# Kernel tuning notes

Measured on AMD Instinct MI355X. Metric: run time of the kernel, lower is better.

## Reference

```python
import jax, jax.numpy as jnp
import numpy as np

B, P, T = 64, 49, 20      # batch, num_pixels (7x7), caption length
V, E, D, A, ENC = 32000, 512, 512, 512, 2048


def setup_inputs() -> dict:
    key = jax.random.key(0)
    ks = jax.random.split(key, 20)
    s = 0.02
    return {
        "features": jax.random.normal(ks[0], (B, P, ENC), jnp.float32),
        "captions": jax.random.randint(ks[1], (B, T), 0, V, jnp.int64),
        "embed_table": jax.random.normal(ks[2], (V, E), jnp.float32) * s,
        "W_ih": jax.random.normal(ks[3], (4 * D, ENC + E), jnp.float32) * s,
        "b_ih": jnp.zeros((4 * D,), jnp.float32),
        "W_hh": jax.random.normal(ks[4], (4 * D, D), jnp.float32) * s,
        "b_hh": jnp.zeros((4 * D,), jnp.float32),
        "W_init_h": jax.random.normal(ks[5], (ENC, D), jnp.float32) * s,
        "b_init_h": jnp.zeros((D,), jnp.float32),
        "W_init_c": jax.random.normal(ks[6], (ENC, D), jnp.float32) * s,
        "b_init_c": jnp.zeros((D,), jnp.float32),
        "W_enc_att": jax.random.normal(ks[7], (ENC, A), jnp.float32) * s,
        "b_enc_att": jnp.zeros((A,), jnp.float32),
        "W_dec_att": jax.random.normal(ks[8], (D, A), jnp.float32) * s,
        "b_dec_att": jnp.zeros((A,), jnp.float32),
        "w_A": jax.random.normal(ks[9], (A,), jnp.float32) * s,
        "b_A": jnp.zeros((), jnp.float32),
        "W_out": jax.random.normal(ks[10], (D, V), jnp.float32) * s,
        "b_out": jnp.zeros((V,), jnp.float32),
    }


def reference(features, captions, embed_table, W_ih, b_ih, W_hh, b_hh,
              W_init_h, b_init_h, W_init_c, b_init_c,
              W_enc_att, b_enc_att, W_dec_att, b_dec_att, w_A, b_A,
              W_out, b_out):
    # Dropout is treated as identity (eval mode) for a deterministic baseline.
    bsz, seq_len = captions.shape
    emb = embed_table[captions]                              # [B,T,E]
    mean_f = features.mean(axis=1)                           # [B,ENC]
    h0 = mean_f @ W_init_h + b_init_h                        # [B,D]
    c0 = mean_f @ W_init_c + b_init_c                        # [B,D]
    enc_states = features @ W_enc_att + b_enc_att            # [B,P,A] (precomputed, loop-invariant)

    def step(carry, x_t):
        h, c = carry
        dec = h @ W_dec_att + b_dec_att                      # [B,A]
        comb = jnp.tanh(enc_states + dec[:, None, :])        # [B,P,A]
        scores = comb @ w_A + b_A                            # [B,P]
        alpha = jax.nn.softmax(scores, axis=1)
        ctx = jnp.einsum('bpe,bp->be', features, alpha)      # [B,ENC]
        x = jnp.concatenate([ctx, x_t], axis=1)              # [B,ENC+E]
        gates = x @ W_ih.T + b_ih + h @ W_hh.T + b_hh        # [B,4D]
        i, f, g, o = jnp.split(gates, 4, axis=1)
        i, f, o = jax.nn.sigmoid(i), jax.nn.sigmoid(f), jax.nn.sigmoid(o)
        g = jnp.tanh(g)
        c2 = f * c + i * g
        h2 = o * jnp.tanh(c2)
        logits = h2 @ W_out + b_out                          # [B,V]
        return (h2, c2), logits

    xs = jnp.swapaxes(emb[:, :seq_len - 1], 0, 1)            # [T-1,B,E]
    _, preds = jax.lax.scan(step, (h0, c0), xs)              # [T-1,B,V]
    preds = jnp.swapaxes(preds, 0, 1)                        # [B,T-1,V]
    vocab = W_out.shape[1]
    last = jnp.zeros((bsz, 1, vocab), preds.dtype)           # t = T-1 never written
    return jnp.concatenate([preds, last], axis=1)            # [B,T,V]
```

## Files before the change

### kernel.cpp

```cpp
#include <hip/hip_runtime.h>

constexpr int B_   = 64;
constexpr int P_   = 49;
constexpr int T_   = 20;
constexpr int V_   = 32000;
constexpr int E_   = 512;
constexpr int D_   = 512;
constexpr int A_   = 512;
constexpr int ENC_ = 2048;
constexpr int NT_  = T_ - 1;
constexpr int KX_  = ENC_ + E_ + D_;
constexpr int KSPL = 8;
constexpr int GCH  = (KX_ / 64) / KSPL;

#define DI __device__ __forceinline__

using u16 = unsigned short;
typedef short   bf16x8 __attribute__((ext_vector_type(8)));
typedef float   f32x4  __attribute__((ext_vector_type(4)));
typedef u16     u16x4  __attribute__((ext_vector_type(4)));
typedef u16     u16x2  __attribute__((ext_vector_type(2)));

DI float sigm(float x) { return 1.0f / (1.0f + __expf(-x)); }
DI float tanhx(float x) {
  x = fminf(15.0f, fmaxf(-15.0f, x));
  float e = __expf(2.0f * x);
  return (e - 1.0f) / (e + 1.0f);
}
DI u16 f2bf(float x) {
  union { float f; unsigned u; } v{x};
  unsigned r = v.u + 0x7FFF + ((v.u >> 16) & 1);
  return (u16)(r >> 16);
}
DI float bf2f(u16 x) {
  union { unsigned u; float f; } v;
  v.u = ((unsigned)x) << 16;
  return v.f;
}
DI f32x4 mfma16(bf16x8 a, bf16x8 b, f32x4 c) {
  return __builtin_amdgcn_mfma_f32_16x16x32_bf16(a, b, c, 0, 0, 0);
}


__global__ __launch_bounds__(256) void k_mean_bf(const float* __restrict__ feat,
                                                 u16* __restrict__ mfb) {
  int idx = blockIdx.x * 256 + threadIdx.x;
  int b = idx >> 11, e = idx & (ENC_ - 1);
  const float* f = feat + (size_t)b * P_ * ENC_ + e;
  float s = 0.f;
#pragma unroll
  for (int p = 0; p < P_; p++) s += f[(size_t)p * ENC_];
  mfb[idx] = f2bf(s * (1.0f / P_));
}

__global__ __launch_bounds__(256) void k_tr_cvt(const float* __restrict__ in,
    u16* __restrict__ outp, int R, int C) {
  __shared__ float tbuf[32][33];
  int tx = threadIdx.x & 31, ty = threadIdx.x >> 5;
  int c0 = blockIdx.x * 32, r0 = blockIdx.y * 32;
#pragma unroll
  for (int i = 0; i < 4; i++)
    tbuf[ty + 8 * i][tx] = in[(size_t)(r0 + ty + 8 * i) * C + c0 + tx];
  __syncthreads();
#pragma unroll
  for (int i = 0; i < 4; i++)
    outp[(size_t)(c0 + ty + 8 * i) * R + r0 + tx] = f2bf(tbuf[tx][ty + 8 * i]);
}

__global__ __launch_bounds__(256) void k_trW(const float* __restrict__ in,
                                             u16* __restrict__ outp) {
  __shared__ u16 ld[128][264];
  int v0 = blockIdx.x * 128, k0 = blockIdx.y * 256;
  int vf = (threadIdx.x & 31) * 4, kk = threadIdx.x >> 5;
#pragma unroll 4
  for (int p = 0; p < 32; p++) {
    int k = kk + p * 8;
    float4 v = *(const float4*)(in + (size_t)(k0 + k) * V_ + v0 + vf);
    ld[vf + 0][k] = f2bf(v.x);
    ld[vf + 1][k] = f2bf(v.y);
    ld[vf + 2][k] = f2bf(v.z);
    ld[vf + 3][k] = f2bf(v.w);
  }
  __syncthreads();
  int v = threadIdx.x >> 1, h = threadIdx.x & 1;
  u16* op = outp + (size_t)(v0 + v) * D_ + k0 + h * 128;
#pragma unroll
  for (int i = 0; i < 16; i++)
    *(bf16x8*)(op + i * 8) = *(const bf16x8*)(&ld[v][h * 128 + i * 8]);
}

__global__ __launch_bounds__(256) void k_cvt4(const float* __restrict__ in,
                                              u16* __restrict__ o) {
  int i = blockIdx.x * 256 + threadIdx.x;
  float4 v = ((const float4*)in)[i];
  u16x4 r = {f2bf(v.x), f2bf(v.y), f2bf(v.z), f2bf(v.w)};
  ((u16x4*)o)[i] = r;
}

__global__ __launch_bounds__(256) void k_wg4(const float* __restrict__ Wih,
    const float* __restrict__ Whh, u16* __restrict__ Wg) {
  int i = blockIdx.x * 256 + threadIdx.x;
  int j = i / 768, rem = i - j * 768;
  int k = rem * 4;
  const float* src = (k < ENC_ + E_) ? (Wih + (size_t)j * (ENC_ + E_) + k)
                                     : (Whh + (size_t)j * D_ + (k - ENC_ - E_));
  float4 v = *(const float4*)src;
  u16x4 r = {f2bf(v.x), f2bf(v.y), f2bf(v.z), f2bf(v.w)};
  ((u16x4*)Wg)[i] = r;
}

__global__ __launch_bounds__(256) void k_emb_bf(const int* __restrict__ cap,
    const float* __restrict__ tab, u16* __restrict__ embb) {
  int idx = blockIdx.x * 256 + threadIdx.x;
  int e = idx & (E_ - 1);
  int tb = idx >> 9;
  int b = tb & 63, t = tb >> 6;
  embb[idx] = f2bf(tab[(size_t)cap[b * T_ + t] * E_ + e]);
}

__global__ __launch_bounds__(256) void k_zero_last(float* __restrict__ out) {
  int i = blockIdx.x * 256 + threadIdx.x;
  int b = i / 8000, v4 = i - b * 8000;
  float4 z = {0.f, 0.f, 0.f, 0.f};
  *(float4*)(out + ((size_t)b * T_ + (T_ - 1)) * V_ + (size_t)v4 * 4) = z;
}

__global__ __launch_bounds__(256) void k_init_bf(const u16* __restrict__ mfb,
    const u16* __restrict__ WiT, const float* __restrict__ binh,
    const float* __restrict__ binc, u16* __restrict__ hbf, float* __restrict__ c) {
  int wid = threadIdx.x >> 6, lane = threadIdx.x & 63;
  int n0 = blockIdx.x * 64 + wid * 16;
  int l16 = lane & 15, lk = lane >> 4;
  const u16* bp = WiT + (size_t)(n0 + l16) * ENC_ + 8 * lk;
  const u16* ap = mfb + (size_t)l16 * ENC_ + 8 * lk;
  f32x4 acc[4] = {};
#pragma unroll 4
  for (int kc = 0; kc < ENC_; kc += 32) {
    bf16x8 b = *(const bf16x8*)(bp + kc);
#pragma unroll
    for (int mf = 0; mf < 4; mf++) {
      bf16x8 a = *(const bf16x8*)(ap + (size_t)mf * 16 * ENC_ + kc);
      acc[mf] = mfma16(a, b, acc[mf]);
    }
  }
  int n = n0 + l16;
#pragma unroll
  for (int mf = 0; mf < 4; mf++) {
    int m = mf * 16 + 4 * lk;
#pragma unroll
    for (int r = 0; r < 4; r++) {
      float v = acc[mf][r];
      if (n < D_) hbf[(size_t)(m + r) * D_ + n] = f2bf(v + binh[n]);
      else        c[(size_t)(m + r) * D_ + (n - D_)] = v + binc[n - D_];
    }
  }
}


__global__ __launch_bounds__(256) void k_enc_bf(const u16* __restrict__ fb,
    const u16* __restrict__ WeT, const float* __restrict__ benc,
    float* __restrict__ encs) {
  int wid = threadIdx.x >> 6, lane = threadIdx.x & 63;
  int m0 = blockIdx.x * 64, n0 = blockIdx.y * 64 + wid * 16;
  int l16 = lane & 15, lk = lane >> 4;
  const u16* ap = fb + (size_t)(m0 + l16) * ENC_ + 8 * lk;
  const u16* bp = WeT + (size_t)(n0 + l16) * ENC_ + 8 * lk;
  f32x4 acc[4] = {};
#pragma unroll 8
  for (int i = 0; i < ENC_ / 32; i++) {
    int kc = i * 32;
    bf16x8 b = *(const bf16x8*)(bp + kc);
#pragma unroll
    for (int mf = 0; mf < 4; mf++) {
      bf16x8 a = *(const bf16x8*)(ap + (size_t)mf * 16 * ENC_ + kc);
      acc[mf] = mfma16(a, b, acc[mf]);
    }
  }
  float bv = benc[n0 + l16];
#pragma unroll
  for (int mf = 0; mf < 4; mf++) {
    int m = m0 + mf * 16 + 4 * lk;
#pragma unroll
    for (int r = 0; r < 4; r++)
      encs[(size_t)(m + r) * A_ + n0 + l16] = acc[mf][r] + bv;
  }
}

__global__ __launch_bounds__(256) void k_gates_bf(const u16* __restrict__ ctxb,
    const u16* __restrict__ embb, const u16* __restrict__ hbf,
    const u16* __restrict__ Wg, float* __restrict__ gp, int t) {
  int wid = threadIdx.x >> 6, lane = threadIdx.x & 63;
  int j0 = blockIdx.x * 64 + wid * 16;
  int sp = blockIdx.y;
  int l16 = lane & 15, lk = lane >> 4;
  const u16* bp = Wg + (size_t)(j0 + l16) * KX_ + 8 * lk;
  f32x4 acc[4] = {};
#pragma unroll
  for (int i = 0; i < KX_ / KSPL / 32; i++) {
    int kc = sp * (KX_ / KSPL) + i * 32;
    int k = kc + 8 * lk;
    bf16x8 b = *(const bf16x8*)(bp + kc);
#pragma unroll
    for (int mf = 0; mf < 4; mf++) {
      int row = mf * 16 + l16;
      const u16* src;
      if (k < ENC_)            src = ctxb + (size_t)row * ENC_ + k;
      else if (k < ENC_ + E_)  src = embb + ((size_t)t * B_ + row) * E_ + (k - ENC_);
      else                     src = hbf + (size_t)row * D_ + (k - ENC_ - E_);
      bf16x8 a = *(const bf16x8*)src;
      acc[mf] = mfma16(a, b, acc[mf]);
    }
  }
#pragma unroll
  for (int mf = 0; mf < 4; mf++) {
    int m = mf * 16 + 4 * lk;
#pragma unroll
    for (int r = 0; r < 4; r++)
      gp[((size_t)sp * B_ + m + r) * (4 * D_) + j0 + l16] = acc[mf][r];
  }
}

__global__ __launch_bounds__(256) void k_logits_all4(const u16* __restrict__ hall,
    const u16* __restrict__ WoT, const float* __restrict__ bout,
    float* __restrict__ out) {
  __shared__ float tile[64 * 264];
  int L = blockIdx.x;
  int x8 = L & 7, r = L >> 3;
  int g = r / 24, s = r % 24;
  int nt = g * 8 + x8;
  if (nt >= 125 || s >= NT_) return;
  int w = threadIdx.x >> 6, lane = threadIdx.x & 63;
  int l16 = lane & 15, lk = lane >> 4;
  const u16* ap0 = hall + (size_t)s * B_ * D_ + (size_t)l16 * D_ + 8 * lk;
  int ncol0 = nt * 256 + w * 64;
#pragma unroll 1
  for (int ch = 0; ch < 4; ch++) {
    int col = ncol0 + ch * 16 + l16;
    const u16* bp = WoT + (size_t)col * D_ + 8 * lk;
    bf16x8 bfr[16];
#pragma unroll
    for (int kc = 0; kc < 16; kc++) bfr[kc] = *(const bf16x8*)(bp + kc * 32);
    f32x4 acc[4] = {};
#pragma unroll
    for (int kc = 0; kc < 16; kc++) {
#pragma unroll
      for (int mf = 0; mf < 4; mf++) {
        bf16x8 a = *(const bf16x8*)(ap0 + (size_t)mf * 16 * D_ + kc * 32);
        acc[mf] = mfma16(a, bfr[kc], acc[mf]);
      }
    }
    float bv = bout[col];
#pragma unroll
    for (int mf = 0; mf < 4; mf++)
#pragma unroll
      for (int rr = 0; rr < 4; rr++)
        tile[(mf * 16 + 4 * lk + rr) * 264 + w * 64 + ch * 16 + l16] =
            acc[mf][rr] + bv;
  }
  __syncthreads();
  int tr = threadIdx.x >> 2, tc = threadIdx.x & 3;
  float* op = out + ((size_t)tr * T_ + s) * V_ + nt * 256;
  const float* lp = &tile[tr * 264];
#pragma unroll
  for (int j = 0; j < 16; j++) {
    int cc = (tc + j * 4) * 4;
    *(float4*)(op + cc) = *(const float4*)(lp + cc);
  }
}


__global__ __launch_bounds__(512) void k_att3(const u16* __restrict__ featb,
    const float* __restrict__ encs, const u16* __restrict__ WdT,
    const float* __restrict__ bdec, const float* __restrict__ wA,
    const float* __restrict__ bA, const float* __restrict__ gp,
    const float* __restrict__ bih, const float* __restrict__ bhh,
    const float* __restrict__ c_in, float* __restrict__ c_out,
    u16* __restrict__ hbf, u16* __restrict__ hallp, u16* __restrict__ ctxb,
    int do_reduce, int do_att) {
  __shared__ u16 hsb[D_];
  __shared__ float ds[A_];
  __shared__ float sc[P_];
  __shared__ float inv_s;
  int b = blockIdx.x, y = blockIdx.y, tid = threadIdx.x;

  if (do_reduce) {
    int d = tid;
    float g0 = 0, g1 = 0, g2 = 0, g3 = 0;
#pragma unroll
    for (int s = 0; s < KSPL; s++) {
      const float* g = gp + (size_t)(s * B_ + b) * (4 * D_);
      g0 += g[d]; g1 += g[D_ + d]; g2 += g[2 * D_ + d]; g3 += g[3 * D_ + d];
    }
    g0 += bih[d] + bhh[d];
    g1 += bih[D_ + d] + bhh[D_ + d];
    g2 += bih[2 * D_ + d] + bhh[2 * D_ + d];
    g3 += bih[3 * D_ + d] + bhh[3 * D_ + d];
    float iv = sigm(g0), fv = sigm(g1), gv = tanhx(g2), ov = sigm(g3);
    float cv = fmaf(fv, c_in[b * D_ + d], iv * gv);
    float hv = ov * tanhx(cv);
    u16 hb = f2bf(hv);
    hsb[d] = hb;
    if (y == 0) {
      c_out[b * D_ + d] = cv;
      hbf[b * D_ + d] = hb;
      hallp[b * D_ + d] = hb;
    }
  } else {
    hsb[tid] = hbf[b * D_ + tid];
  }
  __syncthreads();
  if (!do_att) return;

  {
    int w = tid >> 6, lane = tid & 63, l16 = lane & 15, lk = lane >> 4;
#pragma unroll
    for (int f = 0; f < 4; f++) {
      int n = w * 64 + f * 16 + l16;
      const u16* bp = WdT + (size_t)n * D_ + 8 * lk;
      f32x4 acc = {};
#pragma unroll
      for (int kc = 0; kc < D_; kc += 32) {
        bf16x8 av = *(const bf16x8*)(hsb + kc + 8 * lk);
        bf16x8 bv = *(const bf16x8*)(bp + kc);
        acc = mfma16(av, bv, acc);
      }
      if (lk == 0) ds[n] = acc[0] + bdec[n];
    }
  }
  __syncthreads();

  int wv_ = tid >> 6, ln = tid & 63;
  float bA0 = bA[0];
  for (int p = wv_; p < P_; p += 8) {
    const float* ep = encs + (size_t)(b * P_ + p) * A_;
    float s = 0.f;
#pragma unroll
    for (int a = ln; a < A_; a += 64) s += tanhx(ep[a] + ds[a]) * wA[a];
#pragma unroll
    for (int off = 32; off; off >>= 1) s += __shfl_down(s, off);
    if (ln == 0) sc[p] = s + bA0;
  }
  __syncthreads();

  if (tid == 0) {
    float mx = -1e30f;
    for (int p = 0; p < P_; p++) mx = fmaxf(mx, sc[p]);
    float sum = 0.f;
    for (int p = 0; p < P_; p++) { float ex = __expf(sc[p] - mx); sc[p] = ex; sum += ex; }
    inv_s = 1.0f / sum;
  }
  __syncthreads();

  {
    float inv = inv_s;
    int e = y * 1024 + tid * 2;
    const u16* fp = featb + (size_t)b * P_ * ENC_ + e;
    float s0 = 0.f, s1 = 0.f;
#pragma unroll
    for (int p = 0; p < P_; p++) {
      u16x2 w = *(const u16x2*)(fp + (size_t)p * ENC_);
      s0 = fmaf(bf2f(w.x), sc[p], s0);
      s1 = fmaf(bf2f(w.y), sc[p], s1);
    }
    u16x2 o = {f2bf(s0 * inv), f2bf(s1 * inv)};
    *(u16x2*)(ctxb + b * ENC_ + e) = o;
  }
}


DI int swz(int row, int slot) { return row * 64 + ((slot ^ (row >> 2)) << 2); }

__global__ __launch_bounds__(256) void k_mean(const float* __restrict__ feat,
                                              float* __restrict__ mf) {
  int idx = blockIdx.x * 256 + threadIdx.x;
  int b = idx >> 11, e = idx & (ENC_ - 1);
  const float* f = feat + (size_t)b * P_ * ENC_ + e;
  float s = 0.f;
#pragma unroll
  for (int p = 0; p < P_; p++) s += f[(size_t)p * ENC_];
  mf[idx] = s * (1.0f / P_);
}

__global__ __launch_bounds__(256) void k_emb(const int* __restrict__ cap,
                                             const float* __restrict__ tab,
                                             float* __restrict__ emb) {
  int idx = blockIdx.x * 256 + threadIdx.x;
  int e  = idx & (E_ - 1);
  int bt = idx >> 9;
  int b = bt / NT_, t = bt - b * NT_;
  int tok = cap[b * T_ + t];
  emb[idx] = tab[(size_t)tok * E_ + e];
}

__global__ __launch_bounds__(256) void k_init(const float* __restrict__ mf,
    const float* __restrict__ Wh, const float* __restrict__ bh,
    const float* __restrict__ Wc, const float* __restrict__ bc,
    float* __restrict__ h, float* __restrict__ c) {
  __shared__ float ms[ENC_];
  int b = blockIdx.y;
  for (int i = threadIdx.x; i < ENC_; i += 256) ms[i] = mf[b * ENC_ + i];
  __syncthreads();
  int d = blockIdx.x * 256 + threadIdx.x;
  const float* W = blockIdx.z ? Wc : Wh;
  float s = (blockIdx.z ? bc : bh)[d];
#pragma unroll 8
  for (int e = 0; e < ENC_; e++) s = fmaf(ms[e], W[(size_t)e * D_ + d], s);
  (blockIdx.z ? c : h)[b * D_ + d] = s;
}

__global__ __launch_bounds__(256) void k_enc(const float* __restrict__ Ag,
    const float* __restrict__ Wg, const float* __restrict__ bias,
    float* __restrict__ Cg) {
  __shared__ float As[64 * 64], Ws[64 * 64];
  int m0 = blockIdx.x * 64, n0 = blockIdx.y * 64;
  int tid = threadIdx.x, tn = tid & 15, tm = tid >> 4;
  float acc[4][4] = {};
#pragma unroll 1
  for (int ch = 0; ch < ENC_ / 64; ch++) {
    int k0 = ch * 64;
    __syncthreads();
#pragma unroll
    for (int q = 0; q < 4; q++) {
      int idx = tid + q * 256;
      int row = idx >> 4, slot = idx & 15;
      *(float4*)&As[swz(row, slot)] =
          *(const float4*)(Ag + (size_t)(m0 + row) * ENC_ + k0 + slot * 4);
      *(float4*)&Ws[swz(row, slot)] =
          *(const float4*)(Wg + (size_t)(k0 + row) * A_ + n0 + slot * 4);
    }
    __syncthreads();
#pragma unroll
    for (int kk = 0; kk < 16; kk++) {
      float4 av[4], wv[4];
#pragma unroll
      for (int i = 0; i < 4; i++) av[i] = *(float4*)&As[swz(4 * tm + i, kk)];
#pragma unroll
      for (int u = 0; u < 4; u++) wv[u] = *(float4*)&Ws[swz(4 * kk + u, tn)];
      const float* wq = (const float*)wv;
#pragma unroll
      for (int i = 0; i < 4; i++) {
        const float* aq = (const float*)&av[i];
#pragma unroll
        for (int j = 0; j < 4; j++) {
          float s = acc[i][j];
#pragma unroll
          for (int u = 0; u < 4; u++) s = fmaf(aq[u], wq[u * 4 + j], s);
          acc[i][j] = s;
        }
      }
    }
  }
#pragma unroll
  for (int i = 0; i < 4; i++) {
    int m = m0 + 4 * tm + i, n = n0 + 4 * tn;
    float4 bv = *(const float4*)(bias + n);
    float4 o = {acc[i][0] + bv.x, acc[i][1] + bv.y, acc[i][2] + bv.z, acc[i][3] + bv.w};
    *(float4*)(Cg + (size_t)m * A_ + n) = o;
  }
}

__global__ __launch_bounds__(256) void k_logits(const float* __restrict__ h,
    const float* __restrict__ Wout, const float* __restrict__ bout,
    float* __restrict__ out, int t) {
  __shared__ float As[64 * 64], Ws[64 * 64];
  int n0 = blockIdx.x * 64;
  int tid = threadIdx.x, tn = tid & 15, tm = tid >> 4;
  float acc[4][4] = {};
#pragma unroll 1
  for (int ch = 0; ch < D_ / 64; ch++) {
    int k0 = ch * 64;
    __syncthreads();
#pragma unroll
    for (int q = 0; q < 4; q++) {
      int idx = tid + q * 256;
      int row = idx >> 4, slot = idx & 15;
      *(float4*)&As[swz(row, slot)] =
          *(const float4*)(h + (size_t)row * D_ + k0 + slot * 4);
      *(float4*)&Ws[swz(row, slot)] =
          *(const float4*)(Wout + (size_t)(k0 + row) * V_ + n0 + slot * 4);
    }
    __syncthreads();
#pragma unroll
    for (int kk = 0; kk < 16; kk++) {
      float4 av[4], wv[4];
#pragma unroll
      for (int i = 0; i < 4; i++) av[i] = *(float4*)&As[swz(4 * tm + i, kk)];
#pragma unroll
      for (int u = 0; u < 4; u++) wv[u] = *(float4*)&Ws[swz(4 * kk + u, tn)];
      const float* wq = (const float*)wv;
#pragma unroll
      for (int i = 0; i < 4; i++) {
        const float* aq = (const float*)&av[i];
#pragma unroll
        for (int j = 0; j < 4; j++) {
          float s = acc[i][j];
#pragma unroll
          for (int u = 0; u < 4; u++) s = fmaf(aq[u], wq[u * 4 + j], s);
          acc[i][j] = s;
        }
      }
    }
  }
#pragma unroll
  for (int i = 0; i < 4; i++) {
    int m = 4 * tm + i, n = n0 + 4 * tn;
    float4 bv = *(const float4*)(bout + n);
    float4 o = {acc[i][0] + bv.x, acc[i][1] + bv.y, acc[i][2] + bv.z, acc[i][3] + bv.w};
    *(float4*)(out + ((size_t)m * T_ + t) * V_ + n) = o;
  }
}

__global__ __launch_bounds__(256) void k_gates(const float* __restrict__ ctx,
    const float* __restrict__ emb, const float* __restrict__ h,
    const float* __restrict__ Wih, const float* __restrict__ Whh,
    float* __restrict__ gp, int t) {
  __shared__ float As[64 * 64], Ws[64 * 64];
  int n0 = blockIdx.x * 64;
  int sp = blockIdx.y;
  int tid = threadIdx.x, tn = tid & 15, tm = tid >> 4;
  float acc[4][4] = {};
#pragma unroll 1
  for (int ch = 0; ch < GCH; ch++) {
    int k0 = sp * (GCH * 64) + ch * 64;
    __syncthreads();
#pragma unroll
    for (int q = 0; q < 4; q++) {
      int idx = tid + q * 256;
      int row = idx >> 4, slot = idx & 15;
      int k = k0 + slot * 4;
      float4 xv;
      if (k < ENC_)            xv = *(const float4*)(ctx + (size_t)row * ENC_ + k);
      else if (k < ENC_ + E_)  xv = *(const float4*)(emb + ((size_t)row * NT_ + t) * E_ + (k - ENC_));
      else                     xv = *(const float4*)(h + (size_t)row * D_ + (k - ENC_ - E_));
      *(float4*)&As[swz(row, slot)] = xv;
      int j = n0 + row;
      float4 wv2;
      if (k < ENC_ + E_) wv2 = *(const float4*)(Wih + (size_t)j * (ENC_ + E_) + k);
      else               wv2 = *(const float4*)(Whh + (size_t)j * D_ + (k - ENC_ - E_));
      *(float4*)&Ws[swz(row, slot)] = wv2;
    }
    __syncthreads();
#pragma unroll
    for (int kk = 0; kk < 16; kk++) {
      float4 av[4], wv[4];
#pragma unroll
      for (int i = 0; i < 4; i++) av[i] = *(float4*)&As[swz(4 * tm + i, kk)];
#pragma unroll
      for (int j = 0; j < 4; j++) wv[j] = *(float4*)&Ws[swz(4 * tn + j, kk)];
#pragma unroll
      for (int i = 0; i < 4; i++) {
        const float* aq = (const float*)&av[i];
#pragma unroll
        for (int j = 0; j < 4; j++) {
          const float* wqj = (const float*)&wv[j];
          float s = acc[i][j];
#pragma unroll
          for (int u = 0; u < 4; u++) s = fmaf(aq[u], wqj[u], s);
          acc[i][j] = s;
        }
      }
    }
  }
#pragma unroll
  for (int i = 0; i < 4; i++) {
    int b = 4 * tm + i, j = n0 + 4 * tn;
    float4 o = {acc[i][0], acc[i][1], acc[i][2], acc[i][3]};
    *(float4*)(gp + ((size_t)(sp * B_ + b)) * (4 * D_) + j) = o;
  }
}

__global__ __launch_bounds__(512) void k_att(const float* __restrict__ feat,
    const float* __restrict__ encs, const float* __restrict__ Wdec,
    const float* __restrict__ bdec, const float* __restrict__ wA,
    const float* __restrict__ bA, const float* __restrict__ gp,
    const float* __restrict__ bih, const float* __restrict__ bhh,
    float* __restrict__ h, float* __restrict__ c, float* __restrict__ ctx,
    int do_reduce, int do_att) {
  __shared__ float hs[D_];
  __shared__ float ds[A_];
  __shared__ float sc[P_];
  __shared__ float inv_s;
  int b = blockIdx.x, tid = threadIdx.x;

  if (do_reduce) {
    int d = tid;
    float g0 = 0, g1 = 0, g2 = 0, g3 = 0;
#pragma unroll
    for (int s = 0; s < KSPL; s++) {
      const float* g = gp + (size_t)(s * B_ + b) * (4 * D_);
      g0 += g[d]; g1 += g[D_ + d]; g2 += g[2 * D_ + d]; g3 += g[3 * D_ + d];
    }
    g0 += bih[d] + bhh[d];
    g1 += bih[D_ + d] + bhh[D_ + d];
    g2 += bih[2 * D_ + d] + bhh[2 * D_ + d];
    g3 += bih[3 * D_ + d] + bhh[3 * D_ + d];
    float iv = sigm(g0), fv = sigm(g1), gv = tanhx(g2), ov = sigm(g3);
    float cv = fmaf(fv, c[b * D_ + d], iv * gv);
    float hv = ov * tanhx(cv);
    c[b * D_ + d] = cv;
    h[b * D_ + d] = hv;
    hs[d] = hv;
  } else {
    hs[tid] = h[b * D_ + tid];
  }
  __syncthreads();
  if (!do_att) return;

  {
    int a = tid;
    float s = bdec[a];
#pragma unroll 8
    for (int d = 0; d < D_; d++) s = fmaf(hs[d], Wdec[(size_t)d * A_ + a], s);
    ds[a] = s;
  }
  __syncthreads();

  int wv_ = tid >> 6, ln = tid & 63;
  float bA0 = bA[0];
  for (int p = wv_; p < P_; p += 8) {
    const float* ep = encs + (size_t)(b * P_ + p) * A_;
    float s = 0.f;
#pragma unroll
    for (int a = ln; a < A_; a += 64) s += tanhx(ep[a] + ds[a]) * wA[a];
#pragma unroll
    for (int off = 32; off; off >>= 1) s += __shfl_down(s, off);
    if (ln == 0) sc[p] = s + bA0;
  }
  __syncthreads();

  if (tid == 0) {
    float mx = -1e30f;
    for (int p = 0; p < P_; p++) mx = fmaxf(mx, sc[p]);
    float sum = 0.f;
    for (int p = 0; p < P_; p++) { float ex = __expf(sc[p] - mx); sc[p] = ex; sum += ex; }
    inv_s = 1.0f / sum;
  }
  __syncthreads();

  float inv = inv_s;
  for (int e = tid; e < ENC_; e += 512) {
    const float* fp = feat + (size_t)b * P_ * ENC_ + e;
    float s = 0.f;
#pragma unroll
    for (int p = 0; p < P_; p++) s = fmaf(fp[(size_t)p * ENC_], sc[p], s);
    ctx[b * ENC_ + e] = s * inv;
  }
}


extern "C" void kernel_launch(void* const* d_in, const int* in_sizes, int n_in,
                              void* d_out, int out_size, void* d_ws, size_t ws_size,
                              hipStream_t stream) {
  const float* features = (const float*)d_in[0];
  const int*   captions = (const int*)d_in[1];
  const float* table    = (const float*)d_in[2];
  const float* Wih  = (const float*)d_in[3];
  const float* bih  = (const float*)d_in[4];
  const float* Whh  = (const float*)d_in[5];
  const float* bhh  = (const float*)d_in[6];
  const float* Winh = (const float*)d_in[7];
  const float* binh = (const float*)d_in[8];
  const float* Winc = (const float*)d_in[9];
  const float* binc = (const float*)d_in[10];
  const float* Wenc = (const float*)d_in[11];
  const float* benc = (const float*)d_in[12];
  const float* Wdec = (const float*)d_in[13];
  const float* bdec = (const float*)d_in[14];
  const float* wA   = (const float*)d_in[15];
  const float* bA   = (const float*)d_in[16];
  const float* Wout = (const float*)d_in[17];
  const float* bout = (const float*)d_in[18];
  float* out = (float*)d_out;

  constexpr size_t F_ENC = (size_t)B_ * P_ * A_;
  constexpr size_t F_C   = (size_t)B_ * D_;
  constexpr size_t F_GP  = (size_t)KSPL * B_ * 4 * D_;
  constexpr size_t U_WOT = (size_t)V_ * D_;
  constexpr size_t U_WG  = (size_t)(4 * D_) * KX_;
  constexpr size_t U_HBF = (size_t)B_ * D_;
  constexpr size_t U_CTX = (size_t)B_ * ENC_;
  constexpr size_t U_FEAT = (size_t)B_ * P_ * ENC_;
  constexpr size_t U_WET = (size_t)A_ * ENC_;
  constexpr size_t U_EMB = (size_t)NT_ * B_ * E_;
  constexpr size_t U_WDT = (size_t)A_ * D_;
  constexpr size_t U_HALL = (size_t)NT_ * B_ * D_;
  static_assert(U_EMB + U_WDT <= U_WET, "embb+WdT overlay WeT region");
  constexpr size_t NEED_BYTES =
      (F_ENC + 2 * F_C + F_GP) * 4 +
      (U_WOT + U_WG + U_HBF + U_CTX + U_FEAT + U_WET + U_HALL) * 2;

  if (ws_size >= NEED_BYTES) {
    float* ws = (float*)d_ws;
    float* enc_states = ws;
    float* cbuf0  = enc_states + F_ENC;
    float* cbuf1  = cbuf0 + F_C;
    float* gparts = cbuf1 + F_C;
    u16* WoT   = (u16*)(gparts + F_GP);
    u16* Wg    = WoT + U_WOT;
    u16* hbf   = Wg + U_WG;
    u16* ctxb  = hbf + U_HBF;
    u16* featb = ctxb + U_CTX;
    u16* wetr  = featb + U_FEAT;
    u16* WeT   = wetr;
    u16* embb  = wetr;
    u16* WdT   = wetr + U_EMB;
    u16* hall  = wetr + U_WET;
    u16* WiT   = (u16*)gparts;
    u16* mfb   = ctxb;
    float* cb[2] = {cbuf0, cbuf1};

    k_mean_bf<<<512, 256, 0, stream>>>(features, mfb);
    k_tr_cvt<<<dim3(D_ / 32, ENC_ / 32), 256, 0, stream>>>(Winh, WiT, ENC_, D_);
    k_tr_cvt<<<dim3(D_ / 32, ENC_ / 32), 256, 0, stream>>>(Winc, WiT + (size_t)D_ * ENC_, ENC_, D_);
    k_init_bf<<<16, 256, 0, stream>>>(mfb, WiT, binh, binc, hbf, cbuf0);
    k_cvt4<<<(int)(U_FEAT / 4 / 256), 256, 0, stream>>>(features, featb);
    k_tr_cvt<<<dim3(A_ / 32, ENC_ / 32), 256, 0, stream>>>(Wenc, WeT, ENC_, A_);
    k_enc_bf<<<dim3(49, 8), 256, 0, stream>>>(featb, WeT, benc, enc_states);
    k_emb_bf<<<2432, 256, 0, stream>>>(captions, table, embb);
    k_tr_cvt<<<dim3(A_ / 32, D_ / 32), 256, 0, stream>>>(Wdec, WdT, D_, A_);
    k_trW<<<dim3(V_ / 128, D_ / 256), 256, 0, stream>>>(Wout, WoT);
    k_wg4<<<(int)(U_WG / 4 / 256), 256, 0, stream>>>(Wih, Whh, Wg);
    k_zero_last<<<2000, 256, 0, stream>>>(out);

    for (int t = 0; t < NT_; t++) {
      u16* hallp = (t > 0) ? (hall + (size_t)(t - 1) * B_ * D_) : hall;
      const float* cin = cb[(t > 0 ? (t - 1) : 0) & 1];
      float* cout = cb[t & 1];
      k_att3<<<dim3(64, 2), 512, 0, stream>>>(featb, enc_states, WdT, bdec, wA,
                                              bA, gparts, bih, bhh, cin, cout,
                                              hbf, hallp, ctxb, t > 0 ? 1 : 0, 1);
      k_gates_bf<<<dim3(32, KSPL), 256, 0, stream>>>(ctxb, embb, hbf, Wg, gparts, t);
    }
    k_att3<<<dim3(64, 1), 512, 0, stream>>>(featb, enc_states, WdT, bdec, wA,
                                            bA, gparts, bih, bhh,
                                            cb[(NT_ - 1) & 1], cb[NT_ & 1], hbf,
                                            hall + (size_t)(NT_ - 1) * B_ * D_,
                                            ctxb, 1, 0);
    k_logits_all4<<<3072, 256, 0, stream>>>(hall, WoT, bout, out);
  } else {
    float* ws = (float*)d_ws;
    float* enc_states = ws;
    float* mean_f = enc_states + (size_t)B_ * P_ * A_;
    float* emb    = mean_f + (size_t)B_ * ENC_;
    float* h      = emb + (size_t)B_ * NT_ * E_;
    float* c      = h + (size_t)B_ * D_;
    float* ctx    = c + (size_t)B_ * D_;
    float* gparts = ctx + (size_t)B_ * ENC_;

    k_mean<<<512, 256, 0, stream>>>(features, mean_f);
    k_emb<<<2432, 256, 0, stream>>>(captions, table, emb);
    k_init<<<dim3(2, 64, 2), 256, 0, stream>>>(mean_f, Winh, binh, Winc, binc, h, c);
    k_enc<<<dim3(49, 8), 256, 0, stream>>>(features, Wenc, benc, enc_states);
    k_zero_last<<<2000, 256, 0, stream>>>(out);

    for (int t = 0; t < NT_; t++) {
      k_att<<<64, 512, 0, stream>>>(features, enc_states, Wdec, bdec, wA, bA,
                                    gparts, bih, bhh, h, c, ctx, t > 0 ? 1 : 0, 1);
      if (t > 0)
        k_logits<<<500, 256, 0, stream>>>(h, Wout, bout, out, t - 1);
      k_gates<<<dim3(32, KSPL), 256, 0, stream>>>(ctx, emb, h, Wih, Whh, gparts, t);
    }
    k_att<<<64, 512, 0, stream>>>(features, enc_states, Wdec, bdec, wA, bA,
                                  gparts, bih, bhh, h, c, ctx, 1, 0);
    k_logits<<<500, 256, 0, stream>>>(h, Wout, bout, out, NT_ - 1);
  }
}
```

Baseline: 1.208 ms.

## Fuse recurrent loop into persistent cooperative kernel overlapping logits with recurrence

```diff
diff --git a/kernel.cpp b/kernel.cpp
--- a/kernel.cpp
+++ b/kernel.cpp
@@ -1,4 +1,7 @@
 #include <hip/hip_runtime.h>
+#include <hip/hip_cooperative_groups.h>
+
+namespace cg = cooperative_groups;
 
 constexpr int B_   = 64;
 constexpr int P_   = 49;
@@ -156,7 +159,6 @@
   }
 }
 
-
 __global__ __launch_bounds__(256) void k_enc_bf(const u16* __restrict__ fb,
     const u16* __restrict__ WeT, const float* __restrict__ benc,
     float* __restrict__ encs) {
@@ -185,6 +187,217 @@
       encs[(size_t)(m + r) * A_ + n0 + l16] = acc[mf][r] + bv;
   }
 }
+
+
+DI void logits_tile_512(int nt, int s, const u16* __restrict__ hall,
+                        const u16* __restrict__ WoT,
+                        const float* __restrict__ bout,
+                        float* __restrict__ out, float* __restrict__ tile) {
+  int tid = threadIdx.x;
+  int w = tid >> 6, lane = tid & 63, l16 = lane & 15, lk = lane >> 4;
+  const u16* ap0 = hall + (size_t)s * B_ * D_ + (size_t)l16 * D_ + 8 * lk;
+#pragma unroll
+  for (int ch = 0; ch < 2; ch++) {
+    int col = nt * 256 + w * 32 + ch * 16 + l16;
+    const u16* bp = WoT + (size_t)col * D_ + 8 * lk;
+    f32x4 acc[4] = {};
+#pragma unroll
+    for (int kc = 0; kc < 16; kc++) {
+      bf16x8 b = *(const bf16x8*)(bp + kc * 32);
+#pragma unroll
+      for (int mf = 0; mf < 4; mf++) {
+        bf16x8 a = *(const bf16x8*)(ap0 + (size_t)mf * 16 * D_ + kc * 32);
+        acc[mf] = mfma16(a, b, acc[mf]);
+      }
+    }
+    float bv = bout[col];
+#pragma unroll
+    for (int mf = 0; mf < 4; mf++)
+#pragma unroll
+      for (int rr = 0; rr < 4; rr++)
+        tile[(mf * 16 + 4 * lk + rr) * 264 + w * 32 + ch * 16 + l16] =
+            acc[mf][rr] + bv;
+  }
+  __syncthreads();
+  int tr = tid >> 3, tc = tid & 7;
+  float* op = out + ((size_t)tr * T_ + s) * V_ + nt * 256;
+  const float* lp = tile + tr * 264;
+#pragma unroll
+  for (int j = 0; j < 8; j++) {
+    int cc = (tc + j * 8) * 4;
+    *(float4*)(op + cc) = *(const float4*)(lp + cc);
+  }
+}
+
+__global__ __launch_bounds__(512) void k_loop(
+    const u16* __restrict__ featb, const float* __restrict__ encs,
+    const u16* __restrict__ WdT, const float* __restrict__ bdec,
+    const float* __restrict__ wA, const float* __restrict__ bA,
+    float* __restrict__ gparts, const float* __restrict__ bih,
+    const float* __restrict__ bhh, float* __restrict__ cbuf,
+    u16* __restrict__ hbf, u16* __restrict__ hall, u16* __restrict__ ctxb,
+    const u16* __restrict__ embb, const u16* __restrict__ Wg,
+    const u16* __restrict__ WoT, const float* __restrict__ bout,
+    float* __restrict__ out) {
+  cg::grid_group grid = cg::this_grid();
+  __shared__ float tile[64 * 264];
+  __shared__ u16 hsb[D_];
+  __shared__ float ds[A_];
+  __shared__ float sc[P_];
+  __shared__ float inv_s;
+  int bid = blockIdx.x, tid = threadIdx.x;
+
+  for (int t = 0; t < NT_; t++) {
+    if (bid < 64) {
+      int b = bid;
+      if (t > 0) {
+        int d = tid;
+        float g0 = 0, g1 = 0, g2 = 0, g3 = 0;
+#pragma unroll
+        for (int s = 0; s < KSPL; s++) {
+          const float* g = gparts + (size_t)(s * B_ + b) * (4 * D_);
+          g0 += g[d]; g1 += g[D_ + d]; g2 += g[2 * D_ + d]; g3 += g[3 * D_ + d];
+        }
+        g0 += bih[d] + bhh[d];
+        g1 += bih[D_ + d] + bhh[D_ + d];
+        g2 += bih[2 * D_ + d] + bhh[2 * D_ + d];
+        g3 += bih[3 * D_ + d] + bhh[3 * D_ + d];
+        float iv = sigm(g0), fv = sigm(g1), gv = tanhx(g2), ov = sigm(g3);
+        float cv = fmaf(fv, cbuf[b * D_ + d], iv * gv);
+        float hv = ov * tanhx(cv);
+        cbuf[b * D_ + d] = cv;
+        u16 hb = f2bf(hv);
+        hsb[d] = hb;
+        hbf[b * D_ + d] = hb;
+        hall[(size_t)(t - 1) * B_ * D_ + b * D_ + d] = hb;
+      } else {
+        hsb[tid] = hbf[b * D_ + tid];
+      }
+      __syncthreads();
+
+      {
+        int w = tid >> 6, lane = tid & 63, l16 = lane & 15, lk = lane >> 4;
+#pragma unroll
+        for (int f = 0; f < 4; f++) {
+          int n = w * 64 + f * 16 + l16;
+          const u16* bp = WdT + (size_t)n * D_ + 8 * lk;
+          f32x4 acc = {};
+#pragma unroll
+          for (int kc = 0; kc < D_; kc += 32) {
+            bf16x8 av = *(const bf16x8*)(hsb + kc + 8 * lk);
+            bf16x8 bv = *(const bf16x8*)(bp + kc);
+            acc = mfma16(av, bv, acc);
+          }
+          if (lk == 0) ds[n] = acc[0] + bdec[n];
+        }
+      }
+      __syncthreads();
+
+      {
+        int wv_ = tid >> 6, ln = tid & 63;
+        float bA0 = bA[0];
+        for (int p = wv_; p < P_; p += 8) {
+          const float* ep = encs + (size_t)(b * P_ + p) * A_;
+          float s = 0.f;
+#pragma unroll
+          for (int a = ln; a < A_; a += 64) s += tanhx(ep[a] + ds[a]) * wA[a];
+#pragma unroll
+          for (int off = 32; off; off >>= 1) s += __shfl_down(s, off);
+          if (ln == 0) sc[p] = s + bA0;
+        }
+      }
+      __syncthreads();
+      if (tid == 0) {
+        float mx = -1e30f;
+        for (int p = 0; p < P_; p++) mx = fmaxf(mx, sc[p]);
+        float sum = 0.f;
+        for (int p = 0; p < P_; p++) { float ex = __expf(sc[p] - mx); sc[p] = ex; sum += ex; }
+        inv_s = 1.0f / sum;
+      }
+      __syncthreads();
+
+      {
+        float inv = inv_s;
+        int e = tid * 4;
+        const u16* fp = featb + (size_t)b * P_ * ENC_ + e;
+        float s0 = 0.f, s1 = 0.f, s2 = 0.f, s3 = 0.f;
+#pragma unroll
+        for (int p = 0; p < P_; p++) {
+          u16x4 w = *(const u16x4*)(fp + (size_t)p * ENC_);
+          float scp = sc[p];
+          s0 = fmaf(bf2f(w.x), scp, s0);
+          s1 = fmaf(bf2f(w.y), scp, s1);
+          s2 = fmaf(bf2f(w.z), scp, s2);
+          s3 = fmaf(bf2f(w.w), scp, s3);
+        }
+        u16x4 o = {f2bf(s0 * inv), f2bf(s1 * inv), f2bf(s2 * inv), f2bf(s3 * inv)};
+        *(u16x4*)(ctxb + b * ENC_ + e) = o;
+      }
+    } else if (t >= 2 && bid - 64 < 125) {
+      logits_tile_512(bid - 64, t - 2, hall, WoT, bout, out, tile);
+    }
+    grid.sync();
+
+    if (bid < 128) {
+      int wid8 = tid >> 6;
+      int ob = bid * 2 + (wid8 >> 2);
+      int wid = wid8 & 3;
+      int lane = tid & 63;
+      int j0 = (ob & 31) * 64 + wid * 16;
+      int sp = ob >> 5;
+      int l16 = lane & 15, lk = lane >> 4;
+      const u16* bp = Wg + (size_t)(j0 + l16) * KX_ + 8 * lk;
+      f32x4 acc[4] = {};
+#pragma unroll
+      for (int i = 0; i < KX_ / KSPL / 32; i++) {
+        int kc = sp * (KX_ / KSPL) + i * 32;
+        int k = kc + 8 * lk;
+        bf16x8 b = *(const bf16x8*)(bp + kc);
+#pragma unroll
+        for (int mf = 0; mf < 4; mf++) {
+          int row = mf * 16 + l16;
+          const u16* src;
+          if (k < ENC_)            src = ctxb + (size_t)row * ENC_ + k;
+          else if (k < ENC_ + E_)  src = embb + ((size_t)t * B_ + row) * E_ + (k - ENC_);
+          else                     src = hbf + (size_t)row * D_ + (k - ENC_ - E_);
+          bf16x8 a = *(const bf16x8*)src;
+          acc[mf] = mfma16(a, b, acc[mf]);
+        }
+      }
+#pragma unroll
+      for (int mf = 0; mf < 4; mf++) {
+        int m = mf * 16 + 4 * lk;
+#pragma unroll
+        for (int r = 0; r < 4; r++)
+          gparts[((size_t)sp * B_ + m + r) * (4 * D_) + j0 + l16] = acc[mf][r];
+      }
+    }
+    grid.sync();
+  }
+
+  if (bid < 64) {
+    int b = bid, d = tid;
+    float g0 = 0, g1 = 0, g2 = 0, g3 = 0;
+#pragma unroll
+    for (int s = 0; s < KSPL; s++) {
+      const float* g = gparts + (size_t)(s * B_ + b) * (4 * D_);
+      g0 += g[d]; g1 += g[D_ + d]; g2 += g[2 * D_ + d]; g3 += g[3 * D_ + d];
+    }
+    g0 += bih[d] + bhh[d];
+    g1 += bih[D_ + d] + bhh[D_ + d];
+    g2 += bih[2 * D_ + d] + bhh[2 * D_ + d];
+    g3 += bih[3 * D_ + d] + bhh[3 * D_ + d];
+    float iv = sigm(g0), fv = sigm(g1), gv = tanhx(g2), ov = sigm(g3);
+    float cv = fmaf(fv, cbuf[b * D_ + d], iv * gv);
+    float hv = ov * tanhx(cv);
+    hall[(size_t)(NT_ - 1) * B_ * D_ + b * D_ + d] = f2bf(hv);
+  } else if (bid - 64 < 125) {
+    logits_tile_512(bid - 64, NT_ - 2, hall, WoT, bout, out, tile);
+  }
+  grid.sync();
+  if (bid < 125) logits_tile_512(bid, NT_ - 1, hall, WoT, bout, out, tile);
+}
+
 
 __global__ __launch_bounds__(256) void k_gates_bf(const u16* __restrict__ ctxb,
     const u16* __restrict__ embb, const u16* __restrict__ hbf,
@@ -237,16 +450,14 @@
   for (int ch = 0; ch < 4; ch++) {
     int col = ncol0 + ch * 16 + l16;
     const u16* bp = WoT + (size_t)col * D_ + 8 * lk;
-    bf16x8 bfr[16];
-#pragma unroll
-    for (int kc = 0; kc < 16; kc++) bfr[kc] = *(const bf16x8*)(bp + kc * 32);
     f32x4 acc[4] = {};
 #pragma unroll
     for (int kc = 0; kc < 16; kc++) {
+      bf16x8 b = *(const bf16x8*)(bp + kc * 32);
 #pragma unroll
       for (int mf = 0; mf < 4; mf++) {
         bf16x8 a = *(const bf16x8*)(ap0 + (size_t)mf * 16 * D_ + kc * 32);
-        acc[mf] = mfma16(a, bfr[kc], acc[mf]);
+        acc[mf] = mfma16(a, b, acc[mf]);
       }
     }
     float bv = bout[col];
@@ -267,7 +478,6 @@
     *(float4*)(op + cc) = *(const float4*)(lp + cc);
   }
 }
-
 
 __global__ __launch_bounds__(512) void k_att3(const u16* __restrict__ featb,
     const float* __restrict__ encs, const u16* __restrict__ WdT,
@@ -707,7 +917,6 @@
     u16* hall  = wetr + U_WET;
     u16* WiT   = (u16*)gparts;
     u16* mfb   = ctxb;
-    float* cb[2] = {cbuf0, cbuf1};
 
     k_mean_bf<<<512, 256, 0, stream>>>(features, mfb);
     k_tr_cvt<<<dim3(D_ / 32, ENC_ / 32), 256, 0, stream>>>(Winh, WiT, ENC_, D_);
@@ -722,21 +931,34 @@
     k_wg4<<<(int)(U_WG / 4 / 256), 256, 0, stream>>>(Wih, Whh, Wg);
     k_zero_last<<<2000, 256, 0, stream>>>(out);
 
-    for (int t = 0; t < NT_; t++) {
-      u16* hallp = (t > 0) ? (hall + (size_t)(t - 1) * B_ * D_) : hall;
-      const float* cin = cb[(t > 0 ? (t - 1) : 0) & 1];
-      float* cout = cb[t & 1];
-      k_att3<<<dim3(64, 2), 512, 0, stream>>>(featb, enc_states, WdT, bdec, wA,
-                                              bA, gparts, bih, bhh, cin, cout,
-                                              hbf, hallp, ctxb, t > 0 ? 1 : 0, 1);
-      k_gates_bf<<<dim3(32, KSPL), 256, 0, stream>>>(ctxb, embb, hbf, Wg, gparts, t);
-    }
-    k_att3<<<dim3(64, 1), 512, 0, stream>>>(featb, enc_states, WdT, bdec, wA,
-                                            bA, gparts, bih, bhh,
-                                            cb[(NT_ - 1) & 1], cb[NT_ & 1], hbf,
-                                            hall + (size_t)(NT_ - 1) * B_ * D_,
-                                            ctxb, 1, 0);
-    k_logits_all4<<<3072, 256, 0, stream>>>(hall, WoT, bout, out);
+    void* kargs[] = {
+        (void*)&featb, (void*)&enc_states, (void*)&WdT, (void*)&bdec,
+        (void*)&wA, (void*)&bA, (void*)&gparts, (void*)&bih, (void*)&bhh,
+        (void*)&cbuf0, (void*)&hbf, (void*)&hall, (void*)&ctxb, (void*)&embb,
+        (void*)&Wg, (void*)&WoT, (void*)&bout, (void*)&out};
+    hipError_t ce = hipLaunchCooperativeKernel((void*)k_loop, dim3(256),
+                                               dim3(512), kargs, 0, stream);
+    if (ce != hipSuccess) {
+      float* cb[2] = {cbuf0, cbuf1};
+      for (int t = 0; t < NT_; t++) {
+        u16* hallp = (t > 0) ? (hall + (size_t)(t - 1) * B_ * D_) : hall;
+        const float* cin = cb[(t > 0 ? (t - 1) : 0) & 1];
+        float* cout = cb[t & 1];
+        k_att3<<<dim3(64, 2), 512, 0, stream>>>(featb, enc_states, WdT, bdec,
+                                                wA, bA, gparts, bih, bhh, cin,
+                                                cout, hbf, hallp, ctxb,
+                                                t > 0 ? 1 : 0, 1);
+        k_gates_bf<<<dim3(32, KSPL), 256, 0, stream>>>(ctxb, embb, hbf, Wg,
+                                                       gparts, t);
+      }
+      k_att3<<<dim3(64, 1), 512, 0, stream>>>(featb, enc_states, WdT, bdec, wA,
+                                              bA, gparts, bih, bhh,
+                                              cb[(NT_ - 1) & 1], cb[NT_ & 1],
+                                              hbf,
+                                              hall + (size_t)(NT_ - 1) * B_ * D_,
+                                              ctxb, 1, 0);
+      k_logits_all4<<<3072, 256, 0, stream>>>(hall, WoT, bout, out);
+    }
   } else {
     float* ws = (float*)d_ws;
     float* enc_states = ws;
```

Measured after the change: 3.476 ms. 2.88x slower.

## Split fused attention step into reduce, decoder-proj and attention kernels; halve gate K-split

Applied to the files above, without the earlier changes.

```diff
diff --git a/kernel.cpp b/kernel.cpp
--- a/kernel.cpp
+++ b/kernel.cpp
@@ -12,6 +12,7 @@
 constexpr int KX_  = ENC_ + E_ + D_;
 constexpr int KSPL = 8;
 constexpr int GCH  = (KX_ / 64) / KSPL;
+constexpr int KS4  = 4;
 
 #define DI __device__ __forceinline__
 
@@ -19,7 +20,6 @@
 typedef short   bf16x8 __attribute__((ext_vector_type(8)));
 typedef float   f32x4  __attribute__((ext_vector_type(4)));
 typedef u16     u16x4  __attribute__((ext_vector_type(4)));
-typedef u16     u16x2  __attribute__((ext_vector_type(2)));
 
 DI float sigm(float x) { return 1.0f / (1.0f + __expf(-x)); }
 DI float tanhx(float x) {
@@ -156,7 +156,6 @@
   }
 }
 
-
 __global__ __launch_bounds__(256) void k_enc_bf(const u16* __restrict__ fb,
     const u16* __restrict__ WeT, const float* __restrict__ benc,
     float* __restrict__ encs) {
@@ -186,7 +185,107 @@
   }
 }
 
-__global__ __launch_bounds__(256) void k_gates_bf(const u16* __restrict__ ctxb,
+
+__global__ __launch_bounds__(512) void k_red(const float* __restrict__ gp,
+    const float* __restrict__ bih, const float* __restrict__ bhh,
+    float* __restrict__ c, u16* __restrict__ hbf, u16* __restrict__ hallp) {
+  int b = blockIdx.x, d = threadIdx.x;
+  float g0 = 0, g1 = 0, g2 = 0, g3 = 0;
+#pragma unroll
+  for (int s = 0; s < KS4; s++) {
+    const float* g = gp + (size_t)(s * B_ + b) * (4 * D_);
+    g0 += g[d]; g1 += g[D_ + d]; g2 += g[2 * D_ + d]; g3 += g[3 * D_ + d];
+  }
+  g0 += bih[d] + bhh[d];
+  g1 += bih[D_ + d] + bhh[D_ + d];
+  g2 += bih[2 * D_ + d] + bhh[2 * D_ + d];
+  g3 += bih[3 * D_ + d] + bhh[3 * D_ + d];
+  float iv = sigm(g0), fv = sigm(g1), gv = tanhx(g2), ov = sigm(g3);
+  float cv = fmaf(fv, c[b * D_ + d], iv * gv);
+  float hv = ov * tanhx(cv);
+  c[b * D_ + d] = cv;
+  u16 hb = f2bf(hv);
+  hbf[b * D_ + d] = hb;
+  hallp[b * D_ + d] = hb;
+}
+
+__global__ __launch_bounds__(256) void k_dec(const u16* __restrict__ hbf,
+    const u16* __restrict__ WdT, const float* __restrict__ bdec,
+    float* __restrict__ dsg) {
+  int wid = threadIdx.x >> 6, lane = threadIdx.x & 63;
+  int n0 = blockIdx.x * 64 + wid * 16;
+  int l16 = lane & 15, lk = lane >> 4;
+  const u16* bp = WdT + (size_t)(n0 + l16) * D_ + 8 * lk;
+  const u16* ap = hbf + (size_t)l16 * D_ + 8 * lk;
+  f32x4 acc[4] = {};
+#pragma unroll
+  for (int kc = 0; kc < D_; kc += 32) {
+    bf16x8 b = *(const bf16x8*)(bp + kc);
+#pragma unroll
+    for (int mf = 0; mf < 4; mf++) {
+      bf16x8 a = *(const bf16x8*)(ap + (size_t)mf * 16 * D_ + kc);
+      acc[mf] = mfma16(a, b, acc[mf]);
+    }
+  }
+  int n = n0 + l16;
+  float bv = bdec[n];
+#pragma unroll
+  for (int mf = 0; mf < 4; mf++) {
+    int m = mf * 16 + 4 * lk;
+#pragma unroll
+    for (int r = 0; r < 4; r++)
+      dsg[(size_t)(m + r) * A_ + n] = acc[mf][r] + bv;
+  }
+}
+
+__global__ __launch_bounds__(512) void k_att4(const float* __restrict__ encs,
+    const float* __restrict__ dsg, const float* __restrict__ wA,
+    const float* __restrict__ bA, const u16* __restrict__ featb,
+    u16* __restrict__ ctxb) {
+  __shared__ float sc[P_];
+  __shared__ float inv_s;
+  int b = blockIdx.x, tid = threadIdx.x;
+  int wv_ = tid >> 6, ln = tid & 63;
+  float bA0 = bA[0];
+  const float* dsb = dsg + (size_t)b * A_;
+  for (int p = wv_; p < P_; p += 8) {
+    const float* ep = encs + (size_t)(b * P_ + p) * A_;
+    float s = 0.f;
+#pragma unroll
+    for (int a = ln; a < A_; a += 64) s += tanhx(ep[a] + dsb[a]) * wA[a];
+#pragma unroll
+    for (int off = 32; off; off >>= 1) s += __shfl_down(s, off);
+    if (ln == 0) sc[p] = s + bA0;
+  }
+  __syncthreads();
+  if (tid == 0) {
+    float mx = -1e30f;
+    for (int p = 0; p < P_; p++) mx = fmaxf(mx, sc[p]);
+    float sum = 0.f;
+    for (int p = 0; p < P_; p++) { float ex = __expf(sc[p] - mx); sc[p] = ex; sum += ex; }
+    inv_s = 1.0f / sum;
+  }
+  __syncthreads();
+  {
+    float inv = inv_s;
+    int e = tid * 4;
+    const u16* fp = featb + (size_t)b * P_ * ENC_ + e;
+    float s0 = 0.f, s1 = 0.f, s2 = 0.f, s3 = 0.f;
+#pragma unroll
+    for (int p = 0; p < P_; p++) {
+      u16x4 w = *(const u16x4*)(fp + (size_t)p * ENC_);
+      float scp = sc[p];
+      s0 = fmaf(bf2f(w.x), scp, s0);
+      s1 = fmaf(bf2f(w.y), scp, s1);
+      s2 = fmaf(bf2f(w.z), scp, s2);
+      s3 = fmaf(bf2f(w.w), scp, s3);
+    }
+    u16x4 o = {f2bf(s0 * inv), f2bf(s1 * inv), f2bf(s2 * inv), f2bf(s3 * inv)};
+    *(u16x4*)(ctxb + b * ENC_ + e) = o;
+  }
+}
+
+__global__ __launch_bounds__(256) void k_gates4(const u16* __restrict__ ctxb,
     const u16* __restrict__ embb, const u16* __restrict__ hbf,
     const u16* __restrict__ Wg, float* __restrict__ gp, int t) {
   int wid = threadIdx.x >> 6, lane = threadIdx.x & 63;
@@ -196,8 +295,8 @@
   const u16* bp = Wg + (size_t)(j0 + l16) * KX_ + 8 * lk;
   f32x4 acc[4] = {};
 #pragma unroll
-  for (int i = 0; i < KX_ / KSPL / 32; i++) {
-    int kc = sp * (KX_ / KSPL) + i * 32;
+  for (int i = 0; i < KX_ / KS4 / 32; i++) {
+    int kc = sp * (KX_ / KS4) + i * 32;
     int k = kc + 8 * lk;
     bf16x8 b = *(const bf16x8*)(bp + kc);
 #pragma unroll
@@ -219,6 +318,7 @@
       gp[((size_t)sp * B_ + m + r) * (4 * D_) + j0 + l16] = acc[mf][r];
   }
 }
+
 
 __global__ __launch_bounds__(256) void k_logits_all4(const u16* __restrict__ hall,
     const u16* __restrict__ WoT, const float* __restrict__ bout,
@@ -237,16 +337,14 @@
   for (int ch = 0; ch < 4; ch++) {
     int col = ncol0 + ch * 16 + l16;
     const u16* bp = WoT + (size_t)col * D_ + 8 * lk;
-    bf16x8 bfr[16];
-#pragma unroll
-    for (int kc = 0; kc < 16; kc++) bfr[kc] = *(const bf16x8*)(bp + kc * 32);
     f32x4 acc[4] = {};
 #pragma unroll
     for (int kc = 0; kc < 16; kc++) {
+      bf16x8 b = *(const bf16x8*)(bp + kc * 32);
 #pragma unroll
       for (int mf = 0; mf < 4; mf++) {
         bf16x8 a = *(const bf16x8*)(ap0 + (size_t)mf * 16 * D_ + kc * 32);
-        acc[mf] = mfma16(a, bfr[kc], acc[mf]);
+        acc[mf] = mfma16(a, b, acc[mf]);
       }
     }
     float bv = bout[col];
@@ -265,105 +363,6 @@
   for (int j = 0; j < 16; j++) {
     int cc = (tc + j * 4) * 4;
     *(float4*)(op + cc) = *(const float4*)(lp + cc);
-  }
-}
-
-
-__global__ __launch_bounds__(512) void k_att3(const u16* __restrict__ featb,
-    const float* __restrict__ encs, const u16* __restrict__ WdT,
-    const float* __restrict__ bdec, const float* __restrict__ wA,
-    const float* __restrict__ bA, const float* __restrict__ gp,
-    const float* __restrict__ bih, const float* __restrict__ bhh,
-    const float* __restrict__ c_in, float* __restrict__ c_out,
-    u16* __restrict__ hbf, u16* __restrict__ hallp, u16* __restrict__ ctxb,
-    int do_reduce, int do_att) {
-  __shared__ u16 hsb[D_];
-  __shared__ float ds[A_];
-  __shared__ float sc[P_];
-  __shared__ float inv_s;
-  int b = blockIdx.x, y = blockIdx.y, tid = threadIdx.x;
-
-  if (do_reduce) {
-    int d = tid;
-    float g0 = 0, g1 = 0, g2 = 0, g3 = 0;
-#pragma unroll
-    for (int s = 0; s < KSPL; s++) {
-      const float* g = gp + (size_t)(s * B_ + b) * (4 * D_);
-      g0 += g[d]; g1 += g[D_ + d]; g2 += g[2 * D_ + d]; g3 += g[3 * D_ + d];
-    }
-    g0 += bih[d] + bhh[d];
-    g1 += bih[D_ + d] + bhh[D_ + d];
-    g2 += bih[2 * D_ + d] + bhh[2 * D_ + d];
-    g3 += bih[3 * D_ + d] + bhh[3 * D_ + d];
-    float iv = sigm(g0), fv = sigm(g1), gv = tanhx(g2), ov = sigm(g3);
-    float cv = fmaf(fv, c_in[b * D_ + d], iv * gv);
-    float hv = ov * tanhx(cv);
-    u16 hb = f2bf(hv);
-    hsb[d] = hb;
-    if (y == 0) {
-      c_out[b * D_ + d] = cv;
-      hbf[b * D_ + d] = hb;
-      hallp[b * D_ + d] = hb;
-    }
-  } else {
-    hsb[tid] = hbf[b * D_ + tid];
-  }
-  __syncthreads();
-  if (!do_att) return;
-
-  {
-    int w = tid >> 6, lane = tid & 63, l16 = lane & 15, lk = lane >> 4;
-#pragma unroll
-    for (int f = 0; f < 4; f++) {
-      int n = w * 64 + f * 16 + l16;
-      const u16* bp = WdT + (size_t)n * D_ + 8 * lk;
-      f32x4 acc = {};
-#pragma unroll
-      for (int kc = 0; kc < D_; kc += 32) {
-        bf16x8 av = *(const bf16x8*)(hsb + kc + 8 * lk);
-        bf16x8 bv = *(const bf16x8*)(bp + kc);
-        acc = mfma16(av, bv, acc);
-      }
-      if (lk == 0) ds[n] = acc[0] + bdec[n];
-    }
-  }
-  __syncthreads();
-
-  int wv_ = tid >> 6, ln = tid & 63;
-  float bA0 = bA[0];
-  for (int p = wv_; p < P_; p += 8) {
-    const float* ep = encs + (size_t)(b * P_ + p) * A_;
-    float s = 0.f;
-#pragma unroll
-    for (int a = ln; a < A_; a += 64) s += tanhx(ep[a] + ds[a]) * wA[a];
-#pragma unroll
-    for (int off = 32; off; off >>= 1) s += __shfl_down(s, off);
-    if (ln == 0) sc[p] = s + bA0;
-  }
-  __syncthreads();
-
-  if (tid == 0) {
-    float mx = -1e30f;
-    for (int p = 0; p < P_; p++) mx = fmaxf(mx, sc[p]);
-    float sum = 0.f;
-    for (int p = 0; p < P_; p++) { float ex = __expf(sc[p] - mx); sc[p] = ex; sum += ex; }
-    inv_s = 1.0f / sum;
-  }
-  __syncthreads();
-
-  {
-    float inv = inv_s;
-    int e = y * 1024 + tid * 2;
-    const u16* fp = featb + (size_t)b * P_ * ENC_ + e;
-    float s0 = 0.f, s1 = 0.f;
-#pragma unroll
-    for (int p = 0; p < P_; p++) {
-      u16x2 w = *(const u16x2*)(fp + (size_t)p * ENC_);
-      s0 = fmaf(bf2f(w.x), sc[p], s0);
-      s1 = fmaf(bf2f(w.y), sc[p], s1);
-    }
-    u16x2 o = {f2bf(s0 * inv), f2bf(s1 * inv)};
-    *(u16x2*)(ctxb + b * ENC_ + e) = o;
   }
 }
 
@@ -685,6 +684,8 @@
   constexpr size_t U_WDT = (size_t)A_ * D_;
   constexpr size_t U_HALL = (size_t)NT_ * B_ * D_;
   static_assert(U_EMB + U_WDT <= U_WET, "embb+WdT overlay WeT region");
+  static_assert((size_t)KS4 * B_ * 4 * D_ + (size_t)B_ * A_ <= F_GP,
+                "gp(KS4)+dsg fit in gparts region");
   constexpr size_t NEED_BYTES =
       (F_ENC + 2 * F_C + F_GP) * 4 +
       (U_WOT + U_WG + U_HBF + U_CTX + U_FEAT + U_WET + U_HALL) * 2;
@@ -695,6 +696,7 @@
     float* cbuf0  = enc_states + F_ENC;
     float* cbuf1  = cbuf0 + F_C;
     float* gparts = cbuf1 + F_C;
+    float* dsg    = gparts + (size_t)KS4 * B_ * 4 * D_;
     u16* WoT   = (u16*)(gparts + F_GP);
     u16* Wg    = WoT + U_WOT;
     u16* hbf   = Wg + U_WG;
@@ -707,7 +709,6 @@
     u16* hall  = wetr + U_WET;
     u16* WiT   = (u16*)gparts;
     u16* mfb   = ctxb;
-    float* cb[2] = {cbuf0, cbuf1};
 
     k_mean_bf<<<512, 256, 0, stream>>>(features, mfb);
     k_tr_cvt<<<dim3(D_ / 32, ENC_ / 32), 256, 0, stream>>>(Winh, WiT, ENC_, D_);
@@ -723,19 +724,15 @@
     k_zero_last<<<2000, 256, 0, stream>>>(out);
 
     for (int t = 0; t < NT_; t++) {
-      u16* hallp = (t > 0) ? (hall + (size_t)(t - 1) * B_ * D_) : hall;
-      const float* cin = cb[(t > 0 ? (t - 1) : 0) & 1];
-      float* cout = cb[t & 1];
-      k_att3<<<dim3(64, 2), 512, 0, stream>>>(featb, enc_states, WdT, bdec, wA,
-                                              bA, gparts, bih, bhh, cin, cout,
-                                              hbf, hallp, ctxb, t > 0 ? 1 : 0, 1);
-      k_gates_bf<<<dim3(32, KSPL), 256, 0, stream>>>(ctxb, embb, hbf, Wg, gparts, t);
-    }
-    k_att3<<<dim3(64, 1), 512, 0, stream>>>(featb, enc_states, WdT, bdec, wA,
-                                            bA, gparts, bih, bhh,
-                                            cb[(NT_ - 1) & 1], cb[NT_ & 1], hbf,
-                                            hall + (size_t)(NT_ - 1) * B_ * D_,
-                                            ctxb, 1, 0);
+      if (t > 0)
+        k_red<<<64, 512, 0, stream>>>(gparts, bih, bhh, cbuf0, hbf,
+                                      hall + (size_t)(t - 1) * B_ * D_);
+      k_dec<<<8, 256, 0, stream>>>(hbf, WdT, bdec, dsg);
+      k_att4<<<64, 512, 0, stream>>>(enc_states, dsg, wA, bA, featb, ctxb);
+      k_gates4<<<dim3(32, KS4), 256, 0, stream>>>(ctxb, embb, hbf, Wg, gparts, t);
+    }
+    k_red<<<64, 512, 0, stream>>>(gparts, bih, bhh, cbuf0, hbf,
+                                  hall + (size_t)(NT_ - 1) * B_ * D_);
     k_logits_all4<<<3072, 256, 0, stream>>>(hall, WoT, bout, out);
   } else {
     float* ws = (float*)d_ws;
```

New measurement: 1.392 ms. 1.15x slower.
